# Performance work log

Measured on AMD Instinct MI355X. Metric: run time of the kernel, lower is better.

Reference implementation:

```python
import jax, jax.numpy as jnp
import numpy as np

N = 100000
FEAT = 32
RS, RT = 128, 100
BOUND = 1.6
K_A = -2.0 * np.log(0.2)  # thresholds from module-level constants
K_B = -2.0 * np.log(0.8)


def setup_inputs() -> dict:
    key = jax.random.key(0)
    ks = jax.random.split(key, 10)
    pts = jax.random.normal(ks[0], (N, 3), dtype=jnp.float32) * 0.5
    time = jax.random.uniform(ks[1], (N, 1), dtype=jnp.float32)
    # build well-conditioned SPD covariances, then extract the 6 unique entries
    A = jax.random.normal(ks[2], (N, 3, 3), dtype=jnp.float32) * 0.3
    C = A @ jnp.swapaxes(A, 1, 2) + 0.05 * jnp.eye(3, dtype=jnp.float32)
    cov6 = jnp.stack([C[:, 0, 0], C[:, 0, 1], C[:, 0, 2],
                      C[:, 1, 1], C[:, 1, 2], C[:, 2, 2]], axis=-1)
    planes = {}
    shapes = {0: (FEAT, RS, RS), 1: (FEAT, RS, RS), 2: (FEAT, RS, RT),
              3: (FEAT, RS, RS), 4: (FEAT, RS, RT), 5: (FEAT, RS, RT)}
    for i in range(6):
        planes[f'plane{i}'] = jax.random.normal(ks[3 + i], shapes[i], dtype=jnp.float32) * 0.1
    return dict(pts=pts, time=time, cov6=cov6, **planes)


def _cov3x3(c6):
    # [N,6] -> symmetric [N,3,3]
    r0 = jnp.stack([c6[:, 0], c6[:, 1], c6[:, 2]], axis=-1)
    r1 = jnp.stack([c6[:, 1], c6[:, 3], c6[:, 4]], axis=-1)
    r2 = jnp.stack([c6[:, 2], c6[:, 4], c6[:, 5]], axis=-1)
    return jnp.stack([r0, r1, r2], axis=1)


def _structured_samples(pts, cov6):
    # faithful to structured_gaussian_samples (offsets computed under no_grad)
    sg = jax.lax.stop_gradient
    C = _cov3x3(sg(cov6))
    _, V = jnp.linalg.eigh(C)                      # eigenvectors as columns
    normals = V.reshape(-1, 3)                     # rows of V, as in .view(-1,1,3)
    Cinv = jnp.linalg.inv(C)
    Cinv_rep = jnp.repeat(Cinv, 3, axis=0)         # [3N,3,3]
    lam = jnp.einsum('ni,nij,nj->n', normals, Cinv_rep, normals)[:, None]
    p_a = jnp.sqrt(K_A / lam) * normals
    p_b = jnp.sqrt(K_B / lam) * normals
    o = jnp.repeat(sg(pts), 3, axis=0)             # [3N,3]
    x_a = sg((o + p_a).reshape(-1, 3, 3))
    x_b = sg((o + p_b).reshape(-1, 3, 3))
    x_an = sg((o - p_a).reshape(-1, 3, 3))
    x_bn = sg((o - p_b).reshape(-1, 3, 3))
    return jnp.concatenate([pts[:, None, :], x_a, x_b, x_an, x_bn], axis=1)  # [N,13,3]


def _bilinear(plane, coords):
    # plane [F,H,W]; coords [M,2] in [-1,1], coord0 -> W (x), coord1 -> H (y); align_corners=True
    F_, H, W = plane.shape
    x = (coords[:, 0] + 1.0) * 0.5 * (W - 1)
    y = (coords[:, 1] + 1.0) * 0.5 * (H - 1)
    x0 = jnp.floor(x); y0 = jnp.floor(y)
    wx = (x - x0)[:, None]; wy = (y - y0)[:, None]
    x0i = jnp.clip(x0, 0, W - 1).astype(jnp.int32)
    x1i = jnp.clip(x0 + 1, 0, W - 1).astype(jnp.int32)
    y0i = jnp.clip(y0, 0, H - 1).astype(jnp.int32)
    y1i = jnp.clip(y0 + 1, 0, H - 1).astype(jnp.int32)
    v00 = plane[:, y0i, x0i].T  # [M,F]
    v01 = plane[:, y0i, x1i].T
    v10 = plane[:, y1i, x0i].T
    v11 = plane[:, y1i, x1i].T
    return ((1 - wy) * ((1 - wx) * v00 + wx * v01)
            + wy * ((1 - wx) * v10 + wx * v11))


def _forward(pts, time, cov6, planes):
    M = 13
    samples = _structured_samples(pts, cov6)          # [N,13,3]
    t = time * 2.0 - 1.0
    t = jnp.tile(t, (samples.shape[1], 1))            # faithful to time.repeat(13,1)
    aabb_max = jnp.full((3,), BOUND, dtype=pts.dtype)
    aabb_min = jnp.full((3,), -BOUND, dtype=pts.dtype)
    s = (samples - aabb_max) * (2.0 / (aabb_min - aabb_max)) - 1.0  # normalize_aabb
    data = jnp.concatenate([s.reshape(-1, 3), t], axis=-1)  # [13N,4]
    coord_pairs = [(0, 1), (0, 2), (3, 0), (1, 2), (3, 1), (3, 2)]
    space = 1.0
    spacetime = 1.0
    for i, (q, r) in enumerate(coord_pairs):
        feat = _bilinear(planes[i], data[:, (q, r)])  # [13N,F]
        feat = feat.reshape(-1, M, feat.shape[-1]).mean(axis=1)  # [N,F]
        if i in (0, 1, 3):
            space = space * feat
        else:
            spacetime = spacetime * feat
    return space, spacetime


def reference(pts, time, cov6, plane0, plane1, plane2, plane3, plane4, plane5):
    space, spacetime = _forward(pts, time, cov6,
                                [plane0, plane1, plane2, plane3, plane4, plane5])
    coltime = jnp.ones((), dtype=space.dtype)
    return space, spacetime, coltime
```

## Files before the change

kernel.cpp:

```cpp
#include <hip/hip_runtime.h>
#include <hip/hip_fp16.h>
#include <stdint.h>

#define NP 100000
#define PPB 64
#define KA 3.2188758248682006f
#define KB 0.44628710262841953f
#define PSCALE 16.0f

#define SS_DW 131072
#define ST_DW 102400
#define OFF0 0
#define OFF1 (OFF0 + SS_DW)
#define OFF2 (OFF1 + SS_DW)
#define OFF3 (OFF2 + ST_DW)
#define OFF4 (OFF3 + SS_DW)
#define OFF5 (OFF4 + ST_DW)

typedef float v2f __attribute__((ext_vector_type(2)));
typedef __fp16 v2h __attribute__((ext_vector_type(2)));

__device__ __forceinline__ int clampi(int v, int hi){ v = v < 0 ? 0 : v; return v > hi ? hi : v; }

struct Dim { int i0, i1; float fr; };

__device__ __forceinline__ Dim mkdim(float g, int hi){
  float fl = floorf(g);
  Dim d;
  d.fr = g - fl;
  int i = (int)fl;
  d.i0 = clampi(i, hi);
  d.i1 = clampi(i + 1, hi);
  return d;
}

__device__ __forceinline__ __half2 cvt2h(v2f a){
  v2h h = __builtin_amdgcn_cvt_pkrtz(a.x, a.y);
  return __builtin_bit_cast(__half2, h);
}

__device__ __forceinline__ void corner8(uint2 v, __half2 w, __half2* acc){
  acc[0] = __hfma2(cvt2h(__builtin_amdgcn_cvt_pk_f32_fp8((int)v.x, false)), w, acc[0]);
  acc[1] = __hfma2(cvt2h(__builtin_amdgcn_cvt_pk_f32_fp8((int)v.x, true )), w, acc[1]);
  acc[2] = __hfma2(cvt2h(__builtin_amdgcn_cvt_pk_f32_fp8((int)v.y, false)), w, acc[2]);
  acc[3] = __hfma2(cvt2h(__builtin_amdgcn_cvt_pk_f32_fp8((int)v.y, true )), w, acc[3]);
}

__device__ __forceinline__ void bilin4f8(const uint32_t* __restrict__ P,
    int rA, int rB, int xA, int xB,
    __half2 wxg, __half2 wxf, __half2 wyg, __half2 wyf,
    int fp2, __half2* acc){
  uint2 v00 = *reinterpret_cast<const uint2*>(P + ((rA + xA) << 3) + fp2);
  uint2 v01 = *reinterpret_cast<const uint2*>(P + ((rA + xB) << 3) + fp2);
  uint2 v10 = *reinterpret_cast<const uint2*>(P + ((rB + xA) << 3) + fp2);
  uint2 v11 = *reinterpret_cast<const uint2*>(P + ((rB + xB) << 3) + fp2);
  __half2 w00 = __hmul2(wyg, wxg), w01 = __hmul2(wyg, wxf);
  __half2 w10 = __hmul2(wyf, wxg), w11 = __hmul2(wyf, wxf);
  corner8(v00, w00, acc);
  corner8(v01, w01, acc);
  corner8(v10, w10, acc);
  corner8(v11, w11, acc);
}

__device__ __forceinline__ float3 eigvec3(float c00,float c01,float c02,
                                          float c11,float c12,float c22,float lam){
  float m00 = c00 - lam, m11 = c11 - lam, m22 = c22 - lam;
  float ux0 = c01*c12 - c02*m11, uy0 = c02*c01 - m00*c12, uz0 = m00*m11 - c01*c01;
  float ux1 = c01*m22 - c02*c12, uy1 = c02*c02 - m00*m22, uz1 = m00*c12 - c01*c02;
  float ux2 = m11*m22 - c12*c12, uy2 = c12*c02 - c01*m22, uz2 = c01*c12 - m11*c02;
  float n0 = ux0*ux0 + uy0*uy0 + uz0*uz0;
  float n1 = ux1*ux1 + uy1*uy1 + uz1*uz1;
  float n2 = ux2*ux2 + uy2*uy2 + uz2*uz2;
  float ux = ux0, uy = uy0, uz = uz0, nn = n0;
  if (n1 > nn){ ux = ux1; uy = uy1; uz = uz1; nn = n1; }
  if (n2 > nn){ ux = ux2; uy = uy2; uz = uz2; nn = n2; }
  float inv = 1.0f / sqrtf(nn + 1e-45f);
  return make_float3(ux*inv, uy*inv, uz*inv);
}

__global__ __launch_bounds__(256) void wpf_transpose(
    const float* __restrict__ p0, const float* __restrict__ p1,
    const float* __restrict__ p2, const float* __restrict__ p3,
    const float* __restrict__ p4, const float* __restrict__ p5,
    uint32_t* __restrict__ ws, float* __restrict__ coltime)
{
  __shared__ float tile[32][65];
  int plane = blockIdx.y;
  if (plane == 0 && blockIdx.x == 0 && threadIdx.x == 0) coltime[0] = 1.0f;
  const float* src; int off, HW;
  switch (plane){
    case 0:  src = p0; off = OFF0; HW = 16384; break;
    case 1:  src = p1; off = OFF1; HW = 16384; break;
    case 2:  src = p2; off = OFF2; HW = 12800; break;
    case 3:  src = p3; off = OFF3; HW = 16384; break;
    case 4:  src = p4; off = OFF4; HW = 12800; break;
    default: src = p5; off = OFF5; HW = 12800; break;
  }
  int hw0 = blockIdx.x * 64;
  if (hw0 >= HW) return;
  int hwt = threadIdx.x & 63;
  int fq  = threadIdx.x >> 6;
  #pragma unroll
  for (int i = 0; i < 8; ++i){
    int f = fq * 8 + i;
    tile[f][hwt] = src[f * HW + hw0 + hwt];
  }
  __syncthreads();
  int d  = threadIdx.x & 7;
  int h2 = threadIdx.x >> 3;
  #pragma unroll
  for (int i = 0; i < 2; ++i){
    int hl = i * 32 + h2;
    float a = tile[4*d+0][hl] * PSCALE;
    float b = tile[4*d+1][hl] * PSCALE;
    float c = tile[4*d+2][hl] * PSCALE;
    float e = tile[4*d+3][hl] * PSCALE;
    int r = __builtin_amdgcn_cvt_pk_fp8_f32(a, b, 0, false);
    r     = __builtin_amdgcn_cvt_pk_fp8_f32(c, e, r, true);
    ws[off + (hw0 + hl) * 8 + d] = (uint32_t)r;
  }
}

__global__ __launch_bounds__(256, 4) void wpf_main(
    const float* __restrict__ pts, const float* __restrict__ tim,
    const float* __restrict__ cov6, const uint32_t* __restrict__ ws,
    float* __restrict__ out)
{
  __shared__ float4 smp[PPB][13];
  int tidl = threadIdx.x;
  int pbase = blockIdx.x * PPB;

  if (tidl < PPB){
    int pt = pbase + tidl;
    if (pt < NP){
      float px = pts[pt*3+0], py = pts[pt*3+1], pz = pts[pt*3+2];
      float c00 = cov6[pt*6+0], c01 = cov6[pt*6+1], c02 = cov6[pt*6+2];
      float c11 = cov6[pt*6+3], c12 = cov6[pt*6+4], c22 = cov6[pt*6+5];

      float q3 = (c00 + c11 + c22) * (1.0f/3.0f);
      float p1 = c01*c01 + c02*c02 + c12*c12;
      float d00 = c00 - q3, d11 = c11 - q3, d22 = c22 - q3;
      float p2 = d00*d00 + d11*d11 + d22*d22 + 2.0f*p1;
      float pp = sqrtf(p2 * (1.0f/6.0f)) + 1e-30f;
      float pinv = 1.0f / pp;
      float b00 = d00*pinv, b11 = d11*pinv, b22 = d22*pinv;
      float b01 = c01*pinv, b02 = c02*pinv, b12 = c12*pinv;
      float detB = b00*(b11*b22 - b12*b12) - b01*(b01*b22 - b12*b02) + b02*(b01*b12 - b11*b02);
      float r = fminf(1.0f, fmaxf(-1.0f, 0.5f * detB));
      float phi = acosf(r) * (1.0f/3.0f);
      float l2 = q3 + 2.0f*pp*cosf(phi);
      float l0 = q3 + 2.0f*pp*cosf(phi + 2.0943951023931953f);
      float3 v0 = eigvec3(c00,c01,c02,c11,c12,c22, l0);
      float3 v2 = eigvec3(c00,c01,c02,c11,c12,c22, l2);
      float v1x = v2.y*v0.z - v2.z*v0.y;
      float v1y = v2.z*v0.x - v2.x*v0.z;
      float v1z = v2.x*v0.y - v2.y*v0.x;
      float v1inv = 1.0f / sqrtf(v1x*v1x + v1y*v1y + v1z*v1z + 1e-45f);
      v1x *= v1inv; v1y *= v1inv; v1z *= v1inv;

      float nx[3] = { v0.x, v0.y, v0.z };
      float ny[3] = { v1x,  v1y,  v1z  };
      float nz[3] = { v2.x, v2.y, v2.z };

      float A00 = c11*c22 - c12*c12;
      float A01 = c02*c12 - c01*c22;
      float A02 = c01*c12 - c02*c11;
      float A11 = c00*c22 - c02*c02;
      float A12 = c01*c02 - c00*c12;
      float A22 = c00*c11 - c01*c01;
      float det  = c00*A00 + c01*A01 + c02*A02;
      float dinv = 1.0f / det;
      float i00 = A00*dinv, i01 = A01*dinv, i02 = A02*dinv;
      float i11 = A11*dinv, i12 = A12*dinv, i22 = A22*dinv;

      float gpx = fmaf(px, -39.6875f, 63.5f);
      float gpy = fmaf(py, -39.6875f, 63.5f);
      float gpz = fmaf(pz, -39.6875f, 63.5f);
      float axA[3], ayA[3], azA[3], axB[3], ayB[3], azB[3];
      #pragma unroll
      for (int k = 0; k < 3; ++k){
        float a = nx[k], b = ny[k], c = nz[k];
        float lam = i00*a*a + i11*b*b + i22*c*c + 2.0f*(i01*a*b + i02*a*c + i12*b*c);
        float linv = 1.0f / lam;
        float sA = -39.6875f * sqrtf(KA * linv);
        float sB = -39.6875f * sqrtf(KB * linv);
        axA[k] = sA*a; ayA[k] = sA*b; azA[k] = sA*c;
        axB[k] = sB*a; ayB[k] = sB*b; azB[k] = sB*c;
      }

      int tb = (pt * 13) % NP;
      int ti = tb;
      smp[tidl][0] = make_float4(gpx, gpy, gpz, tim[ti] * 99.0f);
      #pragma unroll
      for (int k = 0; k < 3; ++k){
        ti = tb + 1 + k; if (ti >= NP) ti -= NP;
        smp[tidl][1+k]  = make_float4(gpx+axA[k], gpy+ayA[k], gpz+azA[k], tim[ti]*99.0f);
      }
      #pragma unroll
      for (int k = 0; k < 3; ++k){
        ti = tb + 4 + k; if (ti >= NP) ti -= NP;
        smp[tidl][4+k]  = make_float4(gpx+axB[k], gpy+ayB[k], gpz+azB[k], tim[ti]*99.0f);
      }
      #pragma unroll
      for (int k = 0; k < 3; ++k){
        ti = tb + 7 + k; if (ti >= NP) ti -= NP;
        smp[tidl][7+k]  = make_float4(gpx-axA[k], gpy-ayA[k], gpz-azA[k], tim[ti]*99.0f);
      }
      #pragma unroll
      for (int k = 0; k < 3; ++k){
        ti = tb + 10 + k; if (ti >= NP) ti -= NP;
        smp[tidl][10+k] = make_float4(gpx-axB[k], gpy-ayB[k], gpz-azB[k], tim[ti]*99.0f);
      }
    }
  }
  __syncthreads();

  int lp = tidl >> 2, fp = tidl & 3;
  int pt = pbase + lp;
  if (pt >= NP) return;
  int fp2 = fp << 1;

  const uint32_t* __restrict__ w0p = ws + OFF0;
  const uint32_t* __restrict__ w1p = ws + OFF1;
  const uint32_t* __restrict__ w2p = ws + OFF2;
  const uint32_t* __restrict__ w3p = ws + OFF3;
  const uint32_t* __restrict__ w4p = ws + OFF4;
  const uint32_t* __restrict__ w5p = ws + OFF5;

  __half2 acc[6][4];
  __half2 z = __float2half2_rn(0.0f);
  #pragma unroll
  for (int i = 0; i < 6; ++i){ acc[i][0]=z; acc[i][1]=z; acc[i][2]=z; acc[i][3]=z; }

  #pragma unroll 2
  for (int m = 0; m < 13; ++m){
    float4 s = smp[lp][m];
    Dim d0 = mkdim(s.x, 127);
    Dim d1 = mkdim(s.y, 127);
    Dim d2 = mkdim(s.z, 127);
    Dim dt = mkdim(s.w, 99);

    __half2 f0 = __float2half2_rn(d0.fr), g0 = __float2half2_rn(1.0f - d0.fr);
    __half2 f1 = __float2half2_rn(d1.fr), g1 = __float2half2_rn(1.0f - d1.fr);
    __half2 f2 = __float2half2_rn(d2.fr), g2 = __float2half2_rn(1.0f - d2.fr);
    __half2 ft = __float2half2_rn(dt.fr), gt = __float2half2_rn(1.0f - dt.fr);

    int r1a = d1.i0 << 7, r1b = d1.i1 << 7;
    int r2a = d2.i0 << 7, r2b = d2.i1 << 7;
    int q0a = d0.i0 * 100, q0b = d0.i1 * 100;
    int q1a = d1.i0 * 100, q1b = d1.i1 * 100;
    int q2a = d2.i0 * 100, q2b = d2.i1 * 100;

    bilin4f8(w0p, r1a, r1b, d0.i0, d0.i1, g0, f0, g1, f1, fp2, acc[0]);
    bilin4f8(w1p, r2a, r2b, d0.i0, d0.i1, g0, f0, g2, f2, fp2, acc[1]);
    bilin4f8(w2p, q0a, q0b, dt.i0, dt.i1, gt, ft, g0, f0, fp2, acc[2]);
    bilin4f8(w3p, r2a, r2b, d1.i0, d1.i1, g1, f1, g2, f2, fp2, acc[3]);
    bilin4f8(w4p, q1a, q1b, dt.i0, dt.i1, gt, ft, g1, f1, fp2, acc[4]);
    bilin4f8(w5p, q2a, q2b, dt.i0, dt.i1, gt, ft, g2, f2, fp2, acc[5]);
  }

  const float s13 = 1.0f / (13.0f * PSCALE);
  float sp[8], st[8];
  #pragma unroll
  for (int j = 0; j < 4; ++j){
    float2 a0 = __half22float2(acc[0][j]);
    float2 a1 = __half22float2(acc[1][j]);
    float2 a2 = __half22float2(acc[2][j]);
    float2 a3 = __half22float2(acc[3][j]);
    float2 a4 = __half22float2(acc[4][j]);
    float2 a5 = __half22float2(acc[5][j]);
    sp[2*j]   = (a0.x*s13)*(a1.x*s13)*(a3.x*s13);
    sp[2*j+1] = (a0.y*s13)*(a1.y*s13)*(a3.y*s13);
    st[2*j]   = (a2.x*s13)*(a4.x*s13)*(a5.x*s13);
    st[2*j+1] = (a2.y*s13)*(a4.y*s13)*(a5.y*s13);
  }
  float* osp = out + pt*32 + fp*8;
  float* ost = osp + NP*32;
  reinterpret_cast<float4*>(osp)[0] = make_float4(sp[0], sp[1], sp[2], sp[3]);
  reinterpret_cast<float4*>(osp)[1] = make_float4(sp[4], sp[5], sp[6], sp[7]);
  reinterpret_cast<float4*>(ost)[0] = make_float4(st[0], st[1], st[2], st[3]);
  reinterpret_cast<float4*>(ost)[1] = make_float4(st[4], st[5], st[6], st[7]);
}

extern "C" void kernel_launch(void* const* d_in, const int* in_sizes, int n_in,
                              void* d_out, int out_size, void* d_ws, size_t ws_size,
                              hipStream_t stream) {
  (void)in_sizes; (void)n_in; (void)out_size; (void)ws_size;
  const float* pts  = (const float*)d_in[0];
  const float* tim  = (const float*)d_in[1];
  const float* cov6 = (const float*)d_in[2];
  const float* p0 = (const float*)d_in[3];
  const float* p1 = (const float*)d_in[4];
  const float* p2 = (const float*)d_in[5];
  const float* p3 = (const float*)d_in[6];
  const float* p4 = (const float*)d_in[7];
  const float* p5 = (const float*)d_in[8];
  float* out = (float*)d_out;
  uint32_t* ws = (uint32_t*)d_ws;

  dim3 tgrid(256, 6);
  wpf_transpose<<<tgrid, 256, 0, stream>>>(p0, p1, p2, p3, p4, p5, ws, out + 2*NP*32);

  int nblk = (NP + PPB - 1) / PPB;
  wpf_main<<<nblk, 256, 0, stream>>>(pts, tim, cov6, ws, out);
}
```

Measured before the change: 184.9 us.

## Split bilinear corners across lanes with 16-byte loads and shuffle reduction

The per-thread work is reorganized so each thread of a 4-lane point group handles one x-corner (lo or hi) and 16 features using uint4 loads, instead of all four corners for 8 features with uint2 loads. Partial sums from the two x-corner lanes are combined with a shuffle-xor, and only half the lanes write the outputs. It also switches FP8 decoding to the direct scaled fp8-to-f16 conversion builtin when available, dropping the f32 round-trip. This halves the load instruction count and widens each load, at the cost of doubling the accumulator registers per thread, which may reduce occupancy, and adding a shuffle reduction.

```diff
diff --git a/kernel.cpp b/kernel.cpp
--- a/kernel.cpp
+++ b/kernel.cpp
@@ -34,32 +34,37 @@
   return d;
 }
 
-__device__ __forceinline__ __half2 cvt2h(v2f a){
-  v2h h = __builtin_amdgcn_cvt_pkrtz(a.x, a.y);
+template<bool HI>
+__device__ __forceinline__ __half2 dec8(uint32_t w){
+#if __has_builtin(__builtin_amdgcn_cvt_scalef32_pk_f16_fp8)
+  v2h h = __builtin_amdgcn_cvt_scalef32_pk_f16_fp8(w, 1.0f, HI);
   return __builtin_bit_cast(__half2, h);
-}
-
-__device__ __forceinline__ void corner8(uint2 v, __half2 w, __half2* acc){
-  acc[0] = __hfma2(cvt2h(__builtin_amdgcn_cvt_pk_f32_fp8((int)v.x, false)), w, acc[0]);
-  acc[1] = __hfma2(cvt2h(__builtin_amdgcn_cvt_pk_f32_fp8((int)v.x, true )), w, acc[1]);
-  acc[2] = __hfma2(cvt2h(__builtin_amdgcn_cvt_pk_f32_fp8((int)v.y, false)), w, acc[2]);
-  acc[3] = __hfma2(cvt2h(__builtin_amdgcn_cvt_pk_f32_fp8((int)v.y, true )), w, acc[3]);
-}
-
-__device__ __forceinline__ void bilin4f8(const uint32_t* __restrict__ P,
-    int rA, int rB, int xA, int xB,
-    __half2 wxg, __half2 wxf, __half2 wyg, __half2 wyf,
-    int fp2, __half2* acc){
-  uint2 v00 = *reinterpret_cast<const uint2*>(P + ((rA + xA) << 3) + fp2);
-  uint2 v01 = *reinterpret_cast<const uint2*>(P + ((rA + xB) << 3) + fp2);
-  uint2 v10 = *reinterpret_cast<const uint2*>(P + ((rB + xA) << 3) + fp2);
-  uint2 v11 = *reinterpret_cast<const uint2*>(P + ((rB + xB) << 3) + fp2);
-  __half2 w00 = __hmul2(wyg, wxg), w01 = __hmul2(wyg, wxf);
-  __half2 w10 = __hmul2(wyf, wxg), w11 = __hmul2(wyf, wxf);
-  corner8(v00, w00, acc);
-  corner8(v01, w01, acc);
-  corner8(v10, w10, acc);
-  corner8(v11, w11, acc);
+#else
+  v2f f = __builtin_amdgcn_cvt_pk_f32_fp8((int)w, HI);
+  v2h h = __builtin_amdgcn_cvt_pkrtz(f.x, f.y);
+  return __builtin_bit_cast(__half2, h);
+#endif
+}
+
+__device__ __forceinline__ void row8(uint4 v, __half2 w, __half2* acc){
+  acc[0] = __hfma2(dec8<false>(v.x), w, acc[0]);
+  acc[1] = __hfma2(dec8<true >(v.x), w, acc[1]);
+  acc[2] = __hfma2(dec8<false>(v.y), w, acc[2]);
+  acc[3] = __hfma2(dec8<true >(v.y), w, acc[3]);
+  acc[4] = __hfma2(dec8<false>(v.z), w, acc[4]);
+  acc[5] = __hfma2(dec8<true >(v.z), w, acc[5]);
+  acc[6] = __hfma2(dec8<false>(v.w), w, acc[6]);
+  acc[7] = __hfma2(dec8<true >(v.w), w, acc[7]);
+}
+
+__device__ __forceinline__ void bilinpair(const uint4* __restrict__ P,
+    int rA, int rB, int x0, __half2 wx, __half2 wyg, __half2 wyf,
+    int fp, __half2* acc){
+  uint4 vA = P[((rA + x0) << 1) + fp];
+  uint4 vB = P[((rB + x0) << 1) + fp];
+  __half2 wA = __hmul2(wyg, wx), wB = __hmul2(wyf, wx);
+  row8(vA, wA, acc);
+  row8(vB, wB, acc);
 }
 
 __device__ __forceinline__ float3 eigvec3(float c00,float c01,float c02,
@@ -218,19 +223,21 @@
   int lp = tidl >> 2, fp = tidl & 3;
   int pt = pbase + lp;
   if (pt >= NP) return;
-  int fp2 = fp << 1;
-
-  const uint32_t* __restrict__ w0p = ws + OFF0;
-  const uint32_t* __restrict__ w1p = ws + OFF1;
-  const uint32_t* __restrict__ w2p = ws + OFF2;
-  const uint32_t* __restrict__ w3p = ws + OFF3;
-  const uint32_t* __restrict__ w4p = ws + OFF4;
-  const uint32_t* __restrict__ w5p = ws + OFF5;
-
-  __half2 acc[6][4];
+  bool xhi = (fp & 2) != 0;
+
+  const uint4* __restrict__ w0p = reinterpret_cast<const uint4*>(ws + OFF0);
+  const uint4* __restrict__ w1p = reinterpret_cast<const uint4*>(ws + OFF1);
+  const uint4* __restrict__ w2p = reinterpret_cast<const uint4*>(ws + OFF2);
+  const uint4* __restrict__ w3p = reinterpret_cast<const uint4*>(ws + OFF3);
+  const uint4* __restrict__ w4p = reinterpret_cast<const uint4*>(ws + OFF4);
+  const uint4* __restrict__ w5p = reinterpret_cast<const uint4*>(ws + OFF5);
+
+  __half2 acc[6][8];
   __half2 z = __float2half2_rn(0.0f);
   #pragma unroll
-  for (int i = 0; i < 6; ++i){ acc[i][0]=z; acc[i][1]=z; acc[i][2]=z; acc[i][3]=z; }
+  for (int i = 0; i < 6; ++i)
+    #pragma unroll
+    for (int j = 0; j < 8; ++j) acc[i][j] = z;
 
   #pragma unroll 2
   for (int m = 0; m < 13; ++m){
@@ -240,10 +247,17 @@
     Dim d2 = mkdim(s.z, 127);
     Dim dt = mkdim(s.w, 99);
 
-    __half2 f0 = __float2half2_rn(d0.fr), g0 = __float2half2_rn(1.0f - d0.fr);
-    __half2 f1 = __float2half2_rn(d1.fr), g1 = __float2half2_rn(1.0f - d1.fr);
-    __half2 f2 = __float2half2_rn(d2.fr), g2 = __float2half2_rn(1.0f - d2.fr);
-    __half2 ft = __float2half2_rn(dt.fr), gt = __float2half2_rn(1.0f - dt.fr);
+    float f0x = (d0.i0 == d0.i1) ? 0.0f : d0.fr;
+    float f1x = (d1.i0 == d1.i1) ? 0.0f : d1.fr;
+    float ftx = (dt.i0 == dt.i1) ? 0.0f : dt.fr;
+
+    __half2 f0h = __float2half2_rn(d0.fr), g0h = __float2half2_rn(1.0f - d0.fr);
+    __half2 f1h = __float2half2_rn(d1.fr), g1h = __float2half2_rn(1.0f - d1.fr);
+    __half2 f2h = __float2half2_rn(d2.fr), g2h = __float2half2_rn(1.0f - d2.fr);
+
+    __half2 wx0 = __float2half2_rn(xhi ? f0x : 1.0f - f0x);
+    __half2 wx1 = __float2half2_rn(xhi ? f1x : 1.0f - f1x);
+    __half2 wxt = __float2half2_rn(xhi ? ftx : 1.0f - ftx);
 
     int r1a = d1.i0 << 7, r1b = d1.i1 << 7;
     int r2a = d2.i0 << 7, r2b = d2.i1 << 7;
@@ -251,35 +265,46 @@
     int q1a = d1.i0 * 100, q1b = d1.i1 * 100;
     int q2a = d2.i0 * 100, q2b = d2.i1 * 100;
 
-    bilin4f8(w0p, r1a, r1b, d0.i0, d0.i1, g0, f0, g1, f1, fp2, acc[0]);
-    bilin4f8(w1p, r2a, r2b, d0.i0, d0.i1, g0, f0, g2, f2, fp2, acc[1]);
-    bilin4f8(w2p, q0a, q0b, dt.i0, dt.i1, gt, ft, g0, f0, fp2, acc[2]);
-    bilin4f8(w3p, r2a, r2b, d1.i0, d1.i1, g1, f1, g2, f2, fp2, acc[3]);
-    bilin4f8(w4p, q1a, q1b, dt.i0, dt.i1, gt, ft, g1, f1, fp2, acc[4]);
-    bilin4f8(w5p, q2a, q2b, dt.i0, dt.i1, gt, ft, g2, f2, fp2, acc[5]);
-  }
-
-  const float s13 = 1.0f / (13.0f * PSCALE);
-  float sp[8], st[8];
+    bilinpair(w0p, r1a, r1b, d0.i0, wx0, g1h, f1h, fp, acc[0]);
+    bilinpair(w1p, r2a, r2b, d0.i0, wx0, g2h, f2h, fp, acc[1]);
+    bilinpair(w2p, q0a, q0b, dt.i0, wxt, g0h, f0h, fp, acc[2]);
+    bilinpair(w3p, r2a, r2b, d1.i0, wx1, g2h, f2h, fp, acc[3]);
+    bilinpair(w4p, q1a, q1b, dt.i0, wxt, g1h, f1h, fp, acc[4]);
+    bilinpair(w5p, q2a, q2b, dt.i0, wxt, g2h, f2h, fp, acc[5]);
+  }
+
   #pragma unroll
-  for (int j = 0; j < 4; ++j){
-    float2 a0 = __half22float2(acc[0][j]);
-    float2 a1 = __half22float2(acc[1][j]);
-    float2 a2 = __half22float2(acc[2][j]);
-    float2 a3 = __half22float2(acc[3][j]);
-    float2 a4 = __half22float2(acc[4][j]);
-    float2 a5 = __half22float2(acc[5][j]);
-    sp[2*j]   = (a0.x*s13)*(a1.x*s13)*(a3.x*s13);
-    sp[2*j+1] = (a0.y*s13)*(a1.y*s13)*(a3.y*s13);
-    st[2*j]   = (a2.x*s13)*(a4.x*s13)*(a5.x*s13);
-    st[2*j+1] = (a2.y*s13)*(a4.y*s13)*(a5.y*s13);
-  }
-  float* osp = out + pt*32 + fp*8;
-  float* ost = osp + NP*32;
-  reinterpret_cast<float4*>(osp)[0] = make_float4(sp[0], sp[1], sp[2], sp[3]);
-  reinterpret_cast<float4*>(osp)[1] = make_float4(sp[4], sp[5], sp[6], sp[7]);
-  reinterpret_cast<float4*>(ost)[0] = make_float4(st[0], st[1], st[2], st[3]);
-  reinterpret_cast<float4*>(ost)[1] = make_float4(st[4], st[5], st[6], st[7]);
+  for (int i = 0; i < 6; ++i)
+    #pragma unroll
+    for (int j = 0; j < 8; ++j){
+      int o = __shfl_xor(__builtin_bit_cast(int, acc[i][j]), 2);
+      acc[i][j] = __hadd2(acc[i][j], __builtin_bit_cast(__half2, o));
+    }
+
+  if (fp < 2){
+    const float s13 = 1.0f / (13.0f * PSCALE);
+    float sp[16], st[16];
+    #pragma unroll
+    for (int j = 0; j < 8; ++j){
+      float2 a0 = __half22float2(acc[0][j]);
+      float2 a1 = __half22float2(acc[1][j]);
+      float2 a2 = __half22float2(acc[2][j]);
+      float2 a3 = __half22float2(acc[3][j]);
+      float2 a4 = __half22float2(acc[4][j]);
+      float2 a5 = __half22float2(acc[5][j]);
+      sp[2*j]   = (a0.x*s13)*(a1.x*s13)*(a3.x*s13);
+      sp[2*j+1] = (a0.y*s13)*(a1.y*s13)*(a3.y*s13);
+      st[2*j]   = (a2.x*s13)*(a4.x*s13)*(a5.x*s13);
+      st[2*j+1] = (a2.y*s13)*(a4.y*s13)*(a5.y*s13);
+    }
+    float* osp = out + pt*32 + fp*16;
+    float* ost = osp + NP*32;
+    #pragma unroll
+    for (int q = 0; q < 4; ++q){
+      reinterpret_cast<float4*>(osp)[q] = make_float4(sp[4*q], sp[4*q+1], sp[4*q+2], sp[4*q+3]);
+      reinterpret_cast<float4*>(ost)[q] = make_float4(st[4*q], st[4*q+1], st[4*q+2], st[4*q+3]);
+    }
+  }
 }
 
 extern "C" void kernel_launch(void* const* d_in, const int* in_sizes, int n_in,
```

Result: faster. 174.6 us (-5.6%).
